# Kernel tuning notes

Hardware: AMD Instinct MI355X
Metric: run time of the kernel (lower is better)

## Reference

```python
import jax, jax.numpy as jnp
import numpy as np

EPS = 1e-20

def setup_inputs() -> dict:
    key = jax.random.key(0)
    ks = jax.random.split(key, 6)
    B, N, H = 8, 256, 128
    x = jax.random.normal(ks[0], (B, N, H), dtype=jnp.float32)
    edge_gate = jax.random.uniform(ks[1], (B, N, N, H), dtype=jnp.float32)
    mask = jnp.ones((B, N), dtype=jnp.float32)
    s = 1.0 / np.sqrt(H)
    Uw = jax.random.normal(ks[2], (H, H), dtype=jnp.float32) * s
    Ub = jax.random.normal(ks[3], (H,), dtype=jnp.float32) * s
    Vw = jax.random.normal(ks[4], (H, H), dtype=jnp.float32) * s
    Vb = jax.random.normal(ks[5], (H,), dtype=jnp.float32) * s
    return {"x": x, "edge_gate": edge_gate, "mask": mask,
            "Uw": Uw, "Ub": Ub, "Vw": Vw, "Vb": Vb}

def reference(x, edge_gate, mask, Uw, Ub, Vw, Vb):
    # Linear layers: torch nn.Linear computes x @ W^T + b
    Ux = mask[..., None] * (jnp.einsum('bnh,oh->bno', x, Uw) + Ub)   # (B,N,H)
    Vx = mask[..., None] * (jnp.einsum('bnh,oh->bno', x, Vw) + Vb)   # (B,N,H)
    # mask destination nodes (axis 1) and source nodes (axis 2)
    eg = edge_gate * mask[:, :, None, None] * mask[:, None, :, None]  # (B,N,N,H)
    gateVx_sum = jnp.einsum('bijh,bjh->bih', eg, jnp.ones_like(Vx) * 0 + Vx) if False else jnp.sum(eg * Vx[:, None, :, :], axis=2)  # (B,N,H)
    gate_sum = jnp.sum(eg, axis=2)                                   # (B,N,H)
    return Ux + gateVx_sum / (EPS + gate_sum)
```

## Files before the change

kernel.cpp:

```cpp
#include <hip/hip_runtime.h>

#define EPSF 1e-20f


namespace {
constexpr int Bc = 8;
constexpr int Nc = 256;
constexpr int Hc = 128;
constexpr int ROWS = Bc * Nc;
}

__global__ __launch_bounds__(128) void nf_prep(
    const float* __restrict__ x,
    const float* __restrict__ mask,
    const float* __restrict__ Uw,
    const float* __restrict__ Ub,
    const float* __restrict__ Vw,
    const float* __restrict__ Vb,
    float* __restrict__ Ux,
    float* __restrict__ W)
{
    const int h = threadIdx.x;
    const int row0 = blockIdx.x * 4;

    float accu[4] = {0.f, 0.f, 0.f, 0.f};
    float accv[4] = {0.f, 0.f, 0.f, 0.f};

    const float4* uw4 = reinterpret_cast<const float4*>(Uw + (size_t)h * Hc);
    const float4* vw4 = reinterpret_cast<const float4*>(Vw + (size_t)h * Hc);

    for (int k4 = 0; k4 < Hc / 4; ++k4) {
        const float4 u = uw4[k4];
        const float4 v = vw4[k4];
#pragma unroll
        for (int r = 0; r < 4; ++r) {
            const float4 xv = *reinterpret_cast<const float4*>(
                x + (size_t)(row0 + r) * Hc + k4 * 4);
            accu[r] += xv.x * u.x + xv.y * u.y + xv.z * u.z + xv.w * u.w;
            accv[r] += xv.x * v.x + xv.y * v.y + xv.z * v.z + xv.w * v.w;
        }
    }

    const float bu = Ub[h];
    const float bv = Vb[h];
#pragma unroll
    for (int r = 0; r < 4; ++r) {
        const int row = row0 + r;
        const float m = mask[row];
        Ux[(size_t)row * Hc + h] = m * (accu[r] + bu);
        W[(size_t)row * Hc + h] = m * m * (accv[r] + bv);
    }
}

__global__ __launch_bounds__(256) void nf_edge(
    const float* __restrict__ eg,
    const float* __restrict__ mask,
    const float* __restrict__ Ux,
    const float* __restrict__ W,
    float* __restrict__ out)
{
    const int c = threadIdx.x & 31;
    const int g = threadIdx.x >> 5;
    const int blocksPerB = Nc / 8;
    const int b = blockIdx.x / blocksPerB;
    const int i = (blockIdx.x % blocksPerB) * 8 + g;

    const float* __restrict__ egp =
        eg + ((size_t)(b * Nc + i) * Nc) * Hc + c * 4;
    const float* __restrict__ wp = W + (size_t)(b * Nc) * Hc + c * 4;
    const float* __restrict__ mp = mask + (size_t)b * Nc;

    float4 s1 = {0.f, 0.f, 0.f, 0.f};
    float4 s0 = {0.f, 0.f, 0.f, 0.f};

#pragma unroll 4
    for (int j = 0; j < Nc; ++j) {
        const float mj = mp[j];
        const float4 e = *reinterpret_cast<const float4*>(egp + (size_t)j * Hc);
        const float4 w = *reinterpret_cast<const float4*>(wp + (size_t)j * Hc);
        s1.x += e.x * w.x;
        s1.y += e.y * w.y;
        s1.z += e.z * w.z;
        s1.w += e.w * w.w;
        s0.x += e.x * mj;
        s0.y += e.y * mj;
        s0.z += e.z * mj;
        s0.w += e.w * mj;
    }

    const float mi = mp[i];
    const size_t oidx = (size_t)(b * Nc + i) * Hc + c * 4;
    const float4 ux = *reinterpret_cast<const float4*>(Ux + oidx);

    float4 o;
    o.x = ux.x + (mi * s1.x) / (EPSF + mi * s0.x);
    o.y = ux.y + (mi * s1.y) / (EPSF + mi * s0.y);
    o.z = ux.z + (mi * s1.z) / (EPSF + mi * s0.z);
    o.w = ux.w + (mi * s1.w) / (EPSF + mi * s0.w);
    *reinterpret_cast<float4*>(out + oidx) = o;
}

extern "C" void kernel_launch(void* const* d_in, const int* in_sizes, int n_in,
                              void* d_out, int out_size, void* d_ws, size_t ws_size,
                              hipStream_t stream) {
    const float* x    = (const float*)d_in[0];
    const float* eg   = (const float*)d_in[1];
    const float* mask = (const float*)d_in[2];
    const float* Uw   = (const float*)d_in[3];
    const float* Ub   = (const float*)d_in[4];
    const float* Vw   = (const float*)d_in[5];
    const float* Vb   = (const float*)d_in[6];
    float* out = (float*)d_out;

    float* Ux = (float*)d_ws;
    float* W  = Ux + (size_t)ROWS * Hc;

    nf_prep<<<ROWS / 4, 128, 0, stream>>>(x, mask, Uw, Ub, Vw, Vb, Ux, W);
    nf_edge<<<(Bc * Nc) / 8, 256, 0, stream>>>(eg, mask, Ux, W, out);
}
```

Before: 385.8 us.

## Split each edge row's j-reduction across eight warps with shared-memory combine

The edge kernel now assigns one block per destination row (2048 blocks instead of 256). The eight 32-thread groups each handle a strided subset of source nodes j, and their partial sums are combined through shared memory. The mask row is also staged once in shared memory. The aim is more blocks in flight to saturate memory bandwidth on the 128 MB edge_gate stream, at the cost of extra syncs, a shared-memory reduction and more redundant W reads per row.

```diff
diff --git a/kernel.cpp b/kernel.cpp
--- a/kernel.cpp
+++ b/kernel.cpp
@@ -59,23 +59,30 @@
     const float* __restrict__ W,
     float* __restrict__ out)
 {
-    const int c = threadIdx.x & 31;
-    const int g = threadIdx.x >> 5;
-    const int blocksPerB = Nc / 8;
-    const int b = blockIdx.x / blocksPerB;
-    const int i = (blockIdx.x % blocksPerB) * 8 + g;
+    __shared__ float red1[8][Hc];
+    __shared__ float red0[8][Hc];
+    __shared__ float mrow[Nc];
 
-    const float* __restrict__ egp =
-        eg + ((size_t)(b * Nc + i) * Nc) * Hc + c * 4;
-    const float* __restrict__ wp = W + (size_t)(b * Nc) * Hc + c * 4;
-    const float* __restrict__ mp = mask + (size_t)b * Nc;
+    const int tid = threadIdx.x;
+    const int c = tid & 31;
+    const int g = tid >> 5;
+    const int row = blockIdx.x;
+    const int b = row >> 8;
+    const int i = row & (Nc - 1);
+
+    mrow[tid] = mask[b * Nc + tid];
+    __syncthreads();
+
+    const float* __restrict__ egp = eg + (size_t)row * Nc * Hc + c * 4;
+    const float* __restrict__ wp  = W + (size_t)b * Nc * Hc + c * 4;
 
     float4 s1 = {0.f, 0.f, 0.f, 0.f};
     float4 s0 = {0.f, 0.f, 0.f, 0.f};
 
 #pragma unroll 4
-    for (int j = 0; j < Nc; ++j) {
-        const float mj = mp[j];
+    for (int jj = 0; jj < Nc / 8; ++jj) {
+        const int j = jj * 8 + g;
+        const float mj = mrow[j];
         const float4 e = *reinterpret_cast<const float4*>(egp + (size_t)j * Hc);
         const float4 w = *reinterpret_cast<const float4*>(wp + (size_t)j * Hc);
         s1.x += e.x * w.x;
@@ -88,16 +95,22 @@
         s0.w += e.w * mj;
     }
 
-    const float mi = mp[i];
-    const size_t oidx = (size_t)(b * Nc + i) * Hc + c * 4;
-    const float4 ux = *reinterpret_cast<const float4*>(Ux + oidx);
+    *reinterpret_cast<float4*>(&red1[g][c * 4]) = s1;
+    *reinterpret_cast<float4*>(&red0[g][c * 4]) = s0;
+    __syncthreads();
 
-    float4 o;
-    o.x = ux.x + (mi * s1.x) / (EPSF + mi * s0.x);
-    o.y = ux.y + (mi * s1.y) / (EPSF + mi * s0.y);
-    o.z = ux.z + (mi * s1.z) / (EPSF + mi * s0.z);
-    o.w = ux.w + (mi * s1.w) / (EPSF + mi * s0.w);
-    *reinterpret_cast<float4*>(out + oidx) = o;
+    if (tid < Hc) {
+        const int h = tid;
+        float a1 = 0.f, a0 = 0.f;
+#pragma unroll
+        for (int g2 = 0; g2 < 8; ++g2) {
+            a1 += red1[g2][h];
+            a0 += red0[g2][h];
+        }
+        const float mi = mrow[i];
+        const size_t oidx = (size_t)row * Hc + h;
+        out[oidx] = Ux[oidx] + (mi * a1) / (EPSF + mi * a0);
+    }
 }
 
 extern "C" void kernel_launch(void* const* d_in, const int* in_sizes, int n_in,
@@ -116,5 +129,5 @@
     float* W  = Ux + (size_t)ROWS * Hc;
 
     nf_prep<<<ROWS / 4, 128, 0, stream>>>(x, mask, Uw, Ub, Vw, Vb, Ux, W);
-    nf_edge<<<(Bc * Nc) / 8, 256, 0, stream>>>(eg, mask, Ux, W, out);
+    nf_edge<<<ROWS, 256, 0, stream>>>(eg, mask, Ux, W, out);
 }
```

Measured after the change: 382.7 us. About the same (-0.8%).
